# Kernel tuning notes

Measured on AMD Instinct MI355X. Metric: run time of the kernel, lower is better.

The kernel has to match this reference:

```python
import jax, jax.numpy as jnp
import numpy as np
import math

B = 128
STRIDES = (8.0, 16.0, 32.0)
GRIDS = (128, 64, 32)
C_Q = 4
LAMBDA_BBOX = 5.0
LAMBDA_QUALITY = 0.05
FOCAL_ALPHA = 0.25
FOCAL_GAMMA = 2.0
EPS = 1e-6


def setup_inputs() -> dict:
    key = jax.random.key(0)
    ks = jax.random.split(key, 12)
    inp = {}
    for i, (hw, name) in enumerate(zip(GRIDS, ('det_map8', 'det_map16', 'det_map32'))):
        inp[name] = jax.random.normal(ks[i], (B, 5, hw, hw), dtype=jnp.float32)
    for i, (hw, name) in enumerate(zip(GRIDS, ('qual_map8', 'qual_map16', 'qual_map32'))):
        inp[name] = jax.random.normal(ks[3 + i], (B, C_Q, hw, hw), dtype=jnp.float32)
    # realistic GT boxes inside a 1024x1024 image; every 16th sample invalid (x1 < 0)
    x1 = jax.random.uniform(ks[6], (B,), minval=0.0, maxval=600.0)
    y1 = jax.random.uniform(ks[7], (B,), minval=0.0, maxval=600.0)
    w = jax.random.uniform(ks[8], (B,), minval=64.0, maxval=320.0)
    h = jax.random.uniform(ks[9], (B,), minval=64.0, maxval=320.0)
    boxes = jnp.stack([x1, y1, jnp.minimum(x1 + w, 1023.0), jnp.minimum(y1 + h, 1023.0)], axis=1)
    invalid = (jnp.arange(B) % 16) == 0
    boxes = jnp.where(invalid[:, None], -1.0, boxes)
    inp['gt_bboxes'] = boxes.astype(jnp.float32)
    inp['gt_quality'] = jax.random.uniform(ks[10], (B, C_Q), dtype=jnp.float32)
    return inp


def _level_losses(det, qual, stride, gt_bboxes, gt_quality, valid):
    Bn, _, H, W = det.shape
    gy, gx = jnp.meshgrid(jnp.arange(H, dtype=jnp.float32),
                          jnp.arange(W, dtype=jnp.float32), indexing='ij')
    cx = (gx + 0.5) * stride  # [H,W]
    cy = (gy + 0.5) * stride
    x1 = gt_bboxes[:, 0, None, None]
    y1 = gt_bboxes[:, 1, None, None]
    x2 = gt_bboxes[:, 2, None, None]
    y2 = gt_bboxes[:, 3, None, None]
    in_box = (cx > x1) & (cx < x2) & (cy > y1) & (cy < y2) & valid[:, None, None]  # [B,H,W]

    # --- focal loss on conf channel ---
    z = det[:, 0]
    t = in_box.astype(jnp.float32)
    ce = jnp.maximum(z, 0.0) - z * t + jnp.log1p(jnp.exp(-jnp.abs(z)))
    p = jax.nn.sigmoid(z)
    pt = jnp.where(t == 1, p, 1.0 - p)
    a_t = jnp.where(t == 1, FOCAL_ALPHA, 1.0 - FOCAL_ALPHA)
    focal = a_t * (1.0 - pt) ** FOCAL_GAMMA * ce
    conf = (focal * valid[:, None, None].astype(jnp.float32)).mean()

    # --- CIoU on positive cells (vectorized, masked) ---
    pl = jnp.exp(jnp.clip(det[:, 1], -6.0, 6.0)) * stride
    pt_ = jnp.exp(jnp.clip(det[:, 2], -6.0, 6.0)) * stride
    pr = jnp.exp(jnp.clip(det[:, 3], -6.0, 6.0)) * stride
    pb = jnp.exp(jnp.clip(det[:, 4], -6.0, 6.0)) * stride
    # safe GT distances: positive dummy outside the mask to avoid NaN poisoning
    gl = jnp.where(in_box, cx - x1, 1.0)
    gtl = jnp.where(in_box, cy - y1, 1.0)
    gr = jnp.where(in_box, x2 - cx, 1.0)
    gb = jnp.where(in_box, y2 - cy, 1.0)
    pw = pl + pr
    ph = pt_ + pb
    gw = gl + gr
    gh = gtl + gb
    iw = jnp.clip(jnp.minimum(pl, gl) + jnp.minimum(pr, gr), 0.0)
    ih = jnp.clip(jnp.minimum(pt_, gtl) + jnp.minimum(pb, gb), 0.0)
    inter = iw * ih
    union = pw * ph + gw * gh - inter + EPS
    iou = inter / union
    c_w = jnp.maximum(pl, gl) + jnp.maximum(pr, gr)
    c_h = jnp.maximum(pt_, gtl) + jnp.maximum(pb, gb)
    c2 = c_w ** 2 + c_h ** 2 + EPS
    dcx = (pr - pl) / 2.0 - (gr - gl) / 2.0
    dcy = (pb - pt_) / 2.0 - (gb - gtl) / 2.0
    rho2 = dcx ** 2 + dcy ** 2
    v = (4.0 / math.pi ** 2) * (jnp.arctan(gw / (gh + EPS)) - jnp.arctan(pw / (ph + EPS))) ** 2
    alpha_v = jax.lax.stop_gradient(v / (1.0 - iou + v + EPS))
    ciou = 1.0 - iou + rho2 / c2 + alpha_v * v  # [B,H,W]
    npos_b = in_box.sum(axis=(1, 2))  # [B]
    ciou_mean = (ciou * t).sum(axis=(1, 2)) / jnp.maximum(npos_b, 1).astype(jnp.float32)
    has_pos = npos_b > 0
    bbox = jnp.where(has_pos, ciou_mean, 0.0).sum()

    # --- quality BCE at the positive cell closest to box center ---
    bcx = (gt_bboxes[:, 0] + gt_bboxes[:, 2]) / 2.0
    bcy = (gt_bboxes[:, 1] + gt_bboxes[:, 3]) / 2.0
    dist2 = (cx - bcx[:, None, None]) ** 2 + (cy - bcy[:, None, None]) ** 2
    dist2 = jnp.where(in_box, dist2, jnp.inf)
    idx = jnp.argmin(dist2.reshape(Bn, -1), axis=1)  # [B]
    qual_flat = qual.reshape(Bn, qual.shape[1], -1)  # [B,Cq,HW]
    best = jnp.take_along_axis(qual_flat, idx[:, None, None], axis=2)[:, :, 0]  # [B,Cq]
    q_tgt = jnp.clip(gt_quality, 0.05, 0.95)
    bce = -(q_tgt * jax.nn.log_sigmoid(best) + (1.0 - q_tgt) * jax.nn.log_sigmoid(-best))
    qual_loss = jnp.where(has_pos, bce.mean(axis=1), 0.0).sum()

    return conf, bbox, qual_loss, has_pos.sum()


def _stage_a_loss(det_maps, qual_maps, gt_bboxes, gt_quality):
    valid = gt_bboxes[:, 0] >= 0
    total_conf = jnp.float32(0.0)
    total_bbox = jnp.float32(0.0)
    total_qual = jnp.float32(0.0)
    n_pos = jnp.int32(0)
    for det, qual, stride in zip(det_maps, qual_maps, STRIDES):
        c, b_, q, n = _level_losses(det, qual, stride, gt_bboxes, gt_quality, valid)
        total_conf = total_conf + c
        total_bbox = total_bbox + b_
        total_qual = total_qual + q
        n_pos = n_pos + n
    denom = jnp.maximum(n_pos, 1).astype(jnp.float32)
    total_bbox = jnp.where(n_pos > 0, total_bbox / denom, total_bbox)
    total_qual = jnp.where(n_pos > 0, total_qual / denom, total_qual)
    total = total_conf + LAMBDA_BBOX * total_bbox + LAMBDA_QUALITY * total_qual
    return total, total_conf, total_bbox, total_qual


def reference(det_map8, det_map16, det_map32, qual_map8, qual_map16, qual_map32,
              gt_bboxes, gt_quality):
    return _stage_a_loss((det_map8, det_map16, det_map32),
                         (qual_map8, qual_map16, qual_map32),
                         gt_bboxes, gt_quality)
```

## Files before the change

### kernel.cpp

```cpp
#include <hip/hip_runtime.h>
#include <math.h>


#define NBLK 1408
#define N_PB 384

__device__ __forceinline__ float rcpf(float x) { return __builtin_amdgcn_rcpf(x); }

__device__ __forceinline__ float logsigf(float x) {
    return fminf(x, 0.f) - log1pf(expf(-fabsf(x)));
}

__device__ __forceinline__ void proc4(
    const float* __restrict__ det, size_t c0base, int loc, int Wm1, int log2W,
    size_t HW, float stride, float x1, float y1, float x2, float y2,
    float bcx, float bcy,
    float& conf, float& ciou, int& np, unsigned long long& pk)
{
    const int xi = loc & Wm1;
    const int yi = loc >> log2W;
    const float cy = ((float)yi + 0.5f) * stride;

    float cxs[4]; bool inb[4]; bool anyb = false;
    #pragma unroll
    for (int j = 0; j < 4; ++j) {
        cxs[j] = ((float)(xi + j) + 0.5f) * stride;
        inb[j] = (cxs[j] > x1) & (cxs[j] < x2) & (cy > y1) & (cy < y2);
        anyb |= inb[j];
    }

    const float4 d0 = *(const float4*)(det + c0base + (size_t)loc);
    const float zs[4] = { d0.x, d0.y, d0.z, d0.w };
    #pragma unroll
    for (int j = 0; j < 4; ++j) {
        const float z  = zs[j];
        const float e  = __expf(-fabsf(z));
        const float ce = fmaxf(z, 0.f) - (inb[j] ? z : 0.f) + __logf(1.f + e);
        const float inv = rcpf(1.f + e);
        const float p  = (z >= 0.f) ? inv : e * inv;
        const float pt = inb[j] ? p : 1.f - p;
        const float at = inb[j] ? 0.25f : 0.75f;
        const float om = 1.f - pt;
        conf += at * om * om * ce;
    }

    if (__any(anyb)) {
        const float4 d1 = *(const float4*)(det + c0base + HW + (size_t)loc);
        const float4 d2 = *(const float4*)(det + c0base + 2 * HW + (size_t)loc);
        const float4 d3 = *(const float4*)(det + c0base + 3 * HW + (size_t)loc);
        const float4 d4 = *(const float4*)(det + c0base + 4 * HW + (size_t)loc);
        const float ls[4] = { d1.x, d1.y, d1.z, d1.w };
        const float ts[4] = { d2.x, d2.y, d2.z, d2.w };
        const float rs[4] = { d3.x, d3.y, d3.z, d3.w };
        const float bs[4] = { d4.x, d4.y, d4.z, d4.w };
        #pragma unroll
        for (int j = 0; j < 4; ++j) {
            if (!inb[j]) continue;
            const float cx = cxs[j];
            const float pl  = __expf(fminf(fmaxf(ls[j], -6.f), 6.f)) * stride;
            const float pt_ = __expf(fminf(fmaxf(ts[j], -6.f), 6.f)) * stride;
            const float pr  = __expf(fminf(fmaxf(rs[j], -6.f), 6.f)) * stride;
            const float pb  = __expf(fminf(fmaxf(bs[j], -6.f), 6.f)) * stride;
            const float gl  = cx - x1, gtl = cy - y1, gr = x2 - cx, gb = y2 - cy;
            const float pw = pl + pr, ph = pt_ + pb;
            const float gw = gl + gr, gh = gtl + gb;
            const float iw = fmaxf(fminf(pl, gl) + fminf(pr, gr), 0.f);
            const float ih = fmaxf(fminf(pt_, gtl) + fminf(pb, gb), 0.f);
            const float inter = iw * ih;
            const float uni   = pw * ph + gw * gh - inter + 1e-6f;
            const float iou   = inter * rcpf(uni);
            const float cw_ = fmaxf(pl, gl) + fmaxf(pr, gr);
            const float ch_ = fmaxf(pt_, gtl) + fmaxf(pb, gb);
            const float c2  = cw_ * cw_ + ch_ * ch_ + 1e-6f;
            const float dcx = 0.5f * (pr - pl) - 0.5f * (gr - gl);
            const float dcy = 0.5f * (pb - pt_) - 0.5f * (gb - gtl);
            const float rho2 = dcx * dcx + dcy * dcy;
            const float dv = atanf(gw * rcpf(gh + 1e-6f)) - atanf(pw * rcpf(ph + 1e-6f));
            const float v  = (4.f / (float)(M_PI * M_PI)) * dv * dv;
            const float alpha = v * rcpf(1.f - iou + v + 1e-6f);
            ciou += 1.f - iou + rho2 * rcpf(c2) + alpha * v;
            ++np;
            const float ddx = cx - bcx, ddy = cy - bcy;
            const float dist2 = ddx * ddx + ddy * ddy;
            const unsigned long long cand =
                ((unsigned long long)__float_as_uint(dist2) << 32) | (unsigned)(loc + j);
            pk = cand < pk ? cand : pk;
        }
    }
}

__global__ __launch_bounds__(256) void level_k(
    const float* __restrict__ det8, const float* __restrict__ det16, const float* __restrict__ det32,
    const float* __restrict__ gtb,
    unsigned long long* __restrict__ pk_part, float* __restrict__ conf_part,
    float* __restrict__ ciou_part, int* __restrict__ np_part)
{
    const int bid = blockIdx.x;
    int b, base, log2W, nvec;
    const float* det; float stride; float inv_denom; size_t HW;
    if (bid < 1024) {
        b = bid >> 3; base = (bid & 7) * 2048; nvec = 2;
        det = det8;  stride = 8.f;  log2W = 7; HW = 16384; inv_denom = 1.f / 2097152.f;
    } else if (bid < 1280) {
        const int rel = bid - 1024;
        b = rel >> 1; base = (rel & 1) * 2048; nvec = 2;
        det = det16; stride = 16.f; log2W = 6; HW = 4096; inv_denom = 1.f / 524288.f;
    } else {
        b = bid - 1280; base = 0; nvec = 1;
        det = det32; stride = 32.f; log2W = 5; HW = 1024; inv_denom = 1.f / 131072.f;
    }

    const float x1 = gtb[b * 4 + 0];
    if (x1 < 0.f) {
        if (threadIdx.x == 0) {
            conf_part[bid] = 0.f; ciou_part[bid] = 0.f; np_part[bid] = 0;
            pk_part[bid] = ~0ULL;
        }
        return;
    }
    const float y1 = gtb[b * 4 + 1];
    const float x2 = gtb[b * 4 + 2];
    const float y2 = gtb[b * 4 + 3];
    const float bcx = 0.5f * (x1 + x2);
    const float bcy = 0.5f * (y1 + y2);

    const size_t c0base = (size_t)(b * 5) * HW;
    const int Wm1 = (1 << log2W) - 1;

    float conf = 0.f, ciou = 0.f; int np = 0;
    unsigned long long pk = ~0ULL;

    const int loc0 = base + ((int)threadIdx.x << 2);
    proc4(det, c0base, loc0, Wm1, log2W, HW, stride, x1, y1, x2, y2, bcx, bcy,
          conf, ciou, np, pk);
    if (nvec == 2)
        proc4(det, c0base, loc0 + 1024, Wm1, log2W, HW, stride, x1, y1, x2, y2, bcx, bcy,
              conf, ciou, np, pk);
    conf *= inv_denom;

    #pragma unroll
    for (int off = 32; off > 0; off >>= 1) {
        conf += __shfl_down(conf, off);
        ciou += __shfl_down(ciou, off);
        np   += __shfl_down(np, off);
        unsigned long long o = __shfl_down(pk, off);
        pk = o < pk ? o : pk;
    }

    __shared__ float s_conf[4], s_ciou[4];
    __shared__ int   s_np[4];
    __shared__ unsigned long long s_pk[4];
    const int wid = threadIdx.x >> 6;
    if ((threadIdx.x & 63) == 0) {
        s_conf[wid] = conf; s_ciou[wid] = ciou; s_np[wid] = np; s_pk[wid] = pk;
    }
    __syncthreads();
    if (threadIdx.x == 0) {
        conf_part[bid] = s_conf[0] + s_conf[1] + s_conf[2] + s_conf[3];
        ciou_part[bid] = s_ciou[0] + s_ciou[1] + s_ciou[2] + s_ciou[3];
        np_part[bid]   = s_np[0] + s_np[1] + s_np[2] + s_np[3];
        unsigned long long mn = s_pk[0];
        mn = s_pk[1] < mn ? s_pk[1] : mn;
        mn = s_pk[2] < mn ? s_pk[2] : mn;
        mn = s_pk[3] < mn ? s_pk[3] : mn;
        pk_part[bid] = mn;
    }
}

__global__ __launch_bounds__(512) void fin_k(
    const float* __restrict__ q8, const float* __restrict__ q16, const float* __restrict__ q32,
    const float* __restrict__ gtq,
    const unsigned long long* __restrict__ pk_part, const float* __restrict__ conf_part,
    const float* __restrict__ ciou_part, const int* __restrict__ np_part,
    float* __restrict__ out)
{
    __shared__ float sc[512];
    __shared__ float sb[512];
    __shared__ float sq[512];
    __shared__ int   sn[512];
    const int i = threadIdx.x;

    float cp = 0.f;
    for (int j = i; j < NBLK; j += 512) cp += conf_part[j];

    float bb = 0.f, ql = 0.f; int n = 0;
    if (i < N_PB) {
        const int lvl = i >> 7, b = i & 127;
        int first, cnt;
        if (lvl == 0)      { first = b * 8;        cnt = 8; }
        else if (lvl == 1) { first = 1024 + b * 2; cnt = 2; }
        else               { first = 1280 + b;     cnt = 1; }
        float ci = 0.f; int np = 0; unsigned long long mn = ~0ULL;
        for (int k = 0; k < cnt; ++k) {
            ci += ciou_part[first + k];
            np += np_part[first + k];
            const unsigned long long p = pk_part[first + k];
            mn = p < mn ? p : mn;
        }
        if (np > 0) {
            bb = ci / (float)np;
            const unsigned idx = (unsigned)(mn & 0xffffffffULL);
            const float* q; int log2HW;
            if (lvl == 0)      { q = q8;  log2HW = 14; }
            else if (lvl == 1) { q = q16; log2HW = 12; }
            else               { q = q32; log2HW = 10; }
            float s = 0.f;
            #pragma unroll
            for (int c = 0; c < 4; ++c) {
                const float best = q[((size_t)(b * 4 + c) << log2HW) + idx];
                const float qt = fminf(fmaxf(gtq[b * 4 + c], 0.05f), 0.95f);
                s -= qt * logsigf(best) + (1.f - qt) * logsigf(-best);
            }
            ql = 0.25f * s;
            n = 1;
        }
    }
    sc[i] = cp; sb[i] = bb; sq[i] = ql; sn[i] = n;
    __syncthreads();
    #pragma unroll
    for (int off = 256; off > 0; off >>= 1) {
        if (i < off) { sc[i] += sc[i + off]; sb[i] += sb[i + off]; sq[i] += sq[i + off]; sn[i] += sn[i + off]; }
        __syncthreads();
    }
    if (i == 0) {
        const float conf = sc[0];
        const int ntot = sn[0];
        const float denom = fmaxf((float)ntot, 1.f);
        const float tb = (ntot > 0) ? sb[0] / denom : sb[0];
        const float tq = (ntot > 0) ? sq[0] / denom : sq[0];
        out[0] = conf + 5.f * tb + 0.05f * tq;
        out[1] = conf;
        out[2] = tb;
        out[3] = tq;
    }
}

extern "C" void kernel_launch(void* const* d_in, const int* in_sizes, int n_in,
                              void* d_out, int out_size, void* d_ws, size_t ws_size,
                              hipStream_t stream) {
    const float* det8  = (const float*)d_in[0];
    const float* det16 = (const float*)d_in[1];
    const float* det32 = (const float*)d_in[2];
    const float* q8    = (const float*)d_in[3];
    const float* q16   = (const float*)d_in[4];
    const float* q32   = (const float*)d_in[5];
    const float* gtb   = (const float*)d_in[6];
    const float* gtq   = (const float*)d_in[7];
    float* out = (float*)d_out;

    unsigned long long* pk_part = (unsigned long long*)d_ws;
    float* conf_part = (float*)((char*)d_ws + 11264);
    float* ciou_part = (float*)((char*)d_ws + 16896);
    int*   np_part   = (int*)((char*)d_ws + 22528);

    hipLaunchKernelGGL(level_k, dim3(NBLK), dim3(256), 0, stream,
                       det8, det16, det32, gtb, pk_part, conf_part, ciou_part, np_part);
    hipLaunchKernelGGL(fin_k, dim3(1), dim3(512), 0, stream,
                       q8, q16, q32, gtq, pk_part, conf_part, ciou_part, np_part, out);
}
```

Baseline: 22.02 us.

## Fuse final reduction into level kernel via last-block atomic counter

Merges the separate single-block finalize kernel into the main level kernel. Each block increments a global atomic counter after writing its partials, and the last block to finish does the cross-block reduction and quality-loss gather. This removes one kernel launch and the gap between launches, but adds a memset node, a per-block threadfence and atomic, and a serialized tail on the last block. The det loads are also hoisted so both float4 loads are issued before compute.

```diff
diff --git a/kernel.cpp b/kernel.cpp
--- a/kernel.cpp
+++ b/kernel.cpp
@@ -9,12 +9,22 @@
 
 __device__ __forceinline__ float logsigf(float x) {
     return fminf(x, 0.f) - log1pf(expf(-fabsf(x)));
+}
+
+__device__ __forceinline__ float ld_f32(const float* p) {
+    return __hip_atomic_load(p, __ATOMIC_RELAXED, __HIP_MEMORY_SCOPE_AGENT);
+}
+__device__ __forceinline__ int ld_i32(const int* p) {
+    return __hip_atomic_load(p, __ATOMIC_RELAXED, __HIP_MEMORY_SCOPE_AGENT);
+}
+__device__ __forceinline__ unsigned long long ld_u64(const unsigned long long* p) {
+    return __hip_atomic_load(p, __ATOMIC_RELAXED, __HIP_MEMORY_SCOPE_AGENT);
 }
 
 __device__ __forceinline__ void proc4(
     const float* __restrict__ det, size_t c0base, int loc, int Wm1, int log2W,
     size_t HW, float stride, float x1, float y1, float x2, float y2,
-    float bcx, float bcy,
+    float bcx, float bcy, float4 d0,
     float& conf, float& ciou, int& np, unsigned long long& pk)
 {
     const int xi = loc & Wm1;
@@ -29,7 +39,6 @@
         anyb |= inb[j];
     }
 
-    const float4 d0 = *(const float4*)(det + c0base + (size_t)loc);
     const float zs[4] = { d0.x, d0.y, d0.z, d0.w };
     #pragma unroll
     for (int j = 0; j < 4; ++j) {
@@ -89,13 +98,18 @@
     }
 }
 
-__global__ __launch_bounds__(256) void level_k(
+__global__ __launch_bounds__(256) void fused_k(
     const float* __restrict__ det8, const float* __restrict__ det16, const float* __restrict__ det32,
-    const float* __restrict__ gtb,
+    const float* __restrict__ q8, const float* __restrict__ q16, const float* __restrict__ q32,
+    const float* __restrict__ gtb, const float* __restrict__ gtq,
     unsigned long long* __restrict__ pk_part, float* __restrict__ conf_part,
-    float* __restrict__ ciou_part, int* __restrict__ np_part)
+    float* __restrict__ ciou_part, int* __restrict__ np_part,
+    unsigned int* __restrict__ counter,
+    float* __restrict__ out)
 {
-    const int bid = blockIdx.x;
+    const int tid = (int)threadIdx.x;
+    const int bid = (int)blockIdx.x;
+
     int b, base, log2W, nvec;
     const float* det; float stride; float inv_denom; size_t HW;
     if (bid < 1024) {
@@ -110,33 +124,31 @@
         det = det32; stride = 32.f; log2W = 5; HW = 1024; inv_denom = 1.f / 131072.f;
     }
 
-    const float x1 = gtb[b * 4 + 0];
-    if (x1 < 0.f) {
-        if (threadIdx.x == 0) {
-            conf_part[bid] = 0.f; ciou_part[bid] = 0.f; np_part[bid] = 0;
-            pk_part[bid] = ~0ULL;
-        }
-        return;
-    }
-    const float y1 = gtb[b * 4 + 1];
-    const float x2 = gtb[b * 4 + 2];
-    const float y2 = gtb[b * 4 + 3];
-    const float bcx = 0.5f * (x1 + x2);
-    const float bcy = 0.5f * (y1 + y2);
-
-    const size_t c0base = (size_t)(b * 5) * HW;
-    const int Wm1 = (1 << log2W) - 1;
-
     float conf = 0.f, ciou = 0.f; int np = 0;
     unsigned long long pk = ~0ULL;
 
-    const int loc0 = base + ((int)threadIdx.x << 2);
-    proc4(det, c0base, loc0, Wm1, log2W, HW, stride, x1, y1, x2, y2, bcx, bcy,
-          conf, ciou, np, pk);
-    if (nvec == 2)
-        proc4(det, c0base, loc0 + 1024, Wm1, log2W, HW, stride, x1, y1, x2, y2, bcx, bcy,
-              conf, ciou, np, pk);
-    conf *= inv_denom;
+    const float x1 = gtb[b * 4 + 0];
+    if (x1 >= 0.f) {
+        const float y1 = gtb[b * 4 + 1];
+        const float x2 = gtb[b * 4 + 2];
+        const float y2 = gtb[b * 4 + 3];
+        const float bcx = 0.5f * (x1 + x2);
+        const float bcy = 0.5f * (y1 + y2);
+        const size_t c0base = (size_t)(b * 5) * HW;
+        const int Wm1 = (1 << log2W) - 1;
+        const int locA = base + (tid << 2);
+
+        const float4 dA = *(const float4*)(det + c0base + (size_t)locA);
+        float4 dB;
+        if (nvec == 2) dB = *(const float4*)(det + c0base + (size_t)(locA + 1024));
+
+        proc4(det, c0base, locA, Wm1, log2W, HW, stride, x1, y1, x2, y2, bcx, bcy,
+              dA, conf, ciou, np, pk);
+        if (nvec == 2)
+            proc4(det, c0base, locA + 1024, Wm1, log2W, HW, stride, x1, y1, x2, y2, bcx, bcy,
+                  dB, conf, ciou, np, pk);
+        conf *= inv_denom;
+    }
 
     #pragma unroll
     for (int off = 32; off > 0; off >>= 1) {
@@ -150,12 +162,13 @@
     __shared__ float s_conf[4], s_ciou[4];
     __shared__ int   s_np[4];
     __shared__ unsigned long long s_pk[4];
-    const int wid = threadIdx.x >> 6;
-    if ((threadIdx.x & 63) == 0) {
+    __shared__ int s_last;
+    const int wid = tid >> 6;
+    if ((tid & 63) == 0) {
         s_conf[wid] = conf; s_ciou[wid] = ciou; s_np[wid] = np; s_pk[wid] = pk;
     }
     __syncthreads();
-    if (threadIdx.x == 0) {
+    if (tid == 0) {
         conf_part[bid] = s_conf[0] + s_conf[1] + s_conf[2] + s_conf[3];
         ciou_part[bid] = s_ciou[0] + s_ciou[1] + s_ciou[2] + s_ciou[3];
         np_part[bid]   = s_np[0] + s_np[1] + s_np[2] + s_np[3];
@@ -164,72 +177,71 @@
         mn = s_pk[2] < mn ? s_pk[2] : mn;
         mn = s_pk[3] < mn ? s_pk[3] : mn;
         pk_part[bid] = mn;
-    }
-}
-
-__global__ __launch_bounds__(512) void fin_k(
-    const float* __restrict__ q8, const float* __restrict__ q16, const float* __restrict__ q32,
-    const float* __restrict__ gtq,
-    const unsigned long long* __restrict__ pk_part, const float* __restrict__ conf_part,
-    const float* __restrict__ ciou_part, const int* __restrict__ np_part,
-    float* __restrict__ out)
-{
-    __shared__ float sc[512];
-    __shared__ float sb[512];
-    __shared__ float sq[512];
-    __shared__ int   sn[512];
-    const int i = threadIdx.x;
-
-    float cp = 0.f;
-    for (int j = i; j < NBLK; j += 512) cp += conf_part[j];
-
-    float bb = 0.f, ql = 0.f; int n = 0;
-    if (i < N_PB) {
-        const int lvl = i >> 7, b = i & 127;
+        __threadfence();
+        const unsigned int old = __hip_atomic_fetch_add(
+            counter, 1u, __ATOMIC_ACQ_REL, __HIP_MEMORY_SCOPE_AGENT);
+        s_last = (old == (unsigned)(NBLK - 1)) ? 1 : 0;
+    }
+    __syncthreads();
+    if (!s_last) return;
+
+    __shared__ float fc[256], fb[256], fq[256];
+    __shared__ int   fn[256];
+
+    float cacc = 0.f;
+    for (int j = tid; j < NBLK; j += 256) cacc += ld_f32(conf_part + j);
+
+    float bbacc = 0.f, qlacc = 0.f; int nacc = 0;
+    for (int s = tid; s < N_PB; s += 256) {
+        const int lvl = s >> 7, bb_ = s & 127;
         int first, cnt;
-        if (lvl == 0)      { first = b * 8;        cnt = 8; }
-        else if (lvl == 1) { first = 1024 + b * 2; cnt = 2; }
-        else               { first = 1280 + b;     cnt = 1; }
-        float ci = 0.f; int np = 0; unsigned long long mn = ~0ULL;
+        if (lvl == 0)      { first = bb_ * 8;        cnt = 8; }
+        else if (lvl == 1) { first = 1024 + bb_ * 2; cnt = 2; }
+        else               { first = 1280 + bb_;     cnt = 1; }
+        float ci = 0.f; int nps = 0; unsigned long long mn = ~0ULL;
         for (int k = 0; k < cnt; ++k) {
-            ci += ciou_part[first + k];
-            np += np_part[first + k];
-            const unsigned long long p = pk_part[first + k];
+            ci  += ld_f32(ciou_part + first + k);
+            nps += ld_i32(np_part + first + k);
+            const unsigned long long p = ld_u64(pk_part + first + k);
             mn = p < mn ? p : mn;
         }
-        if (np > 0) {
-            bb = ci / (float)np;
+        if (nps > 0) {
+            bbacc += ci / (float)nps;
             const unsigned idx = (unsigned)(mn & 0xffffffffULL);
-            const float* q; int log2HW;
-            if (lvl == 0)      { q = q8;  log2HW = 14; }
-            else if (lvl == 1) { q = q16; log2HW = 12; }
-            else               { q = q32; log2HW = 10; }
-            float s = 0.f;
+            const float* q; int log2HW2;
+            if (lvl == 0)      { q = q8;  log2HW2 = 14; }
+            else if (lvl == 1) { q = q16; log2HW2 = 12; }
+            else               { q = q32; log2HW2 = 10; }
+            float sacc = 0.f;
             #pragma unroll
             for (int c = 0; c < 4; ++c) {
-                const float best = q[((size_t)(b * 4 + c) << log2HW) + idx];
-                const float qt = fminf(fmaxf(gtq[b * 4 + c], 0.05f), 0.95f);
-                s -= qt * logsigf(best) + (1.f - qt) * logsigf(-best);
+                const float best = q[((size_t)(bb_ * 4 + c) << log2HW2) + idx];
+                const float qt = fminf(fmaxf(gtq[bb_ * 4 + c], 0.05f), 0.95f);
+                sacc -= qt * logsigf(best) + (1.f - qt) * logsigf(-best);
             }
-            ql = 0.25f * s;
-            n = 1;
-        }
-    }
-    sc[i] = cp; sb[i] = bb; sq[i] = ql; sn[i] = n;
+            qlacc += 0.25f * sacc;
+            nacc  += 1;
+        }
+    }
+
+    fc[tid] = cacc; fb[tid] = bbacc; fq[tid] = qlacc; fn[tid] = nacc;
     __syncthreads();
     #pragma unroll
-    for (int off = 256; off > 0; off >>= 1) {
-        if (i < off) { sc[i] += sc[i + off]; sb[i] += sb[i + off]; sq[i] += sq[i + off]; sn[i] += sn[i + off]; }
+    for (int off = 128; off > 0; off >>= 1) {
+        if (tid < off) {
+            fc[tid] += fc[tid + off]; fb[tid] += fb[tid + off];
+            fq[tid] += fq[tid + off]; fn[tid] += fn[tid + off];
+        }
         __syncthreads();
     }
-    if (i == 0) {
-        const float conf = sc[0];
-        const int ntot = sn[0];
+    if (tid == 0) {
+        const float conf_t = fc[0];
+        const int ntot = fn[0];
         const float denom = fmaxf((float)ntot, 1.f);
-        const float tb = (ntot > 0) ? sb[0] / denom : sb[0];
-        const float tq = (ntot > 0) ? sq[0] / denom : sq[0];
-        out[0] = conf + 5.f * tb + 0.05f * tq;
-        out[1] = conf;
+        const float tb = (ntot > 0) ? fb[0] / denom : fb[0];
+        const float tq = (ntot > 0) ? fq[0] / denom : fq[0];
+        out[0] = conf_t + 5.f * tb + 0.05f * tq;
+        out[1] = conf_t;
         out[2] = tb;
         out[3] = tq;
     }
@@ -252,9 +264,10 @@
     float* conf_part = (float*)((char*)d_ws + 11264);
     float* ciou_part = (float*)((char*)d_ws + 16896);
     int*   np_part   = (int*)((char*)d_ws + 22528);
-
-    hipLaunchKernelGGL(level_k, dim3(NBLK), dim3(256), 0, stream,
-                       det8, det16, det32, gtb, pk_part, conf_part, ciou_part, np_part);
-    hipLaunchKernelGGL(fin_k, dim3(1), dim3(512), 0, stream,
-                       q8, q16, q32, gtq, pk_part, conf_part, ciou_part, np_part, out);
-}
+    unsigned int* counter = (unsigned int*)((char*)d_ws + 28160);
+
+    hipMemsetAsync(counter, 0, 4, stream);
+    hipLaunchKernelGGL(fused_k, dim3(NBLK), dim3(256), 0, stream,
+                       det8, det16, det32, q8, q16, q32, gtb, gtq,
+                       pk_part, conf_part, ciou_part, np_part, counter, out);
+}
```

Result: slower. 69.56 us (+215.9%).
